# Performance work log

Measured on AMD Instinct MI355X. Metric: run time of the kernel, lower is better.

## Reference

```python
import jax, jax.numpy as jnp
import numpy as np


def median_pool8(x):
    # x: (N, 1, H0, W0); 8x8 non-overlapping blocks, lower median (torch.median semantics)
    N, C, H0, W0 = x.shape
    H, W = H0 // 8, W0 // 8
    blocks = x.reshape(N, C, H, 8, W, 8).transpose(0, 1, 2, 4, 3, 5).reshape(N, C, H, W, 64)
    return jnp.sort(blocks, axis=-1)[..., (64 - 1) // 2]


def prelu(x, a):
    return jnp.where(x >= 0, x, a * x)


def setup_inputs() -> dict:
    key = jax.random.key(0)
    ks = jax.random.split(key, 12)
    N, C, H, W = 8, 128, 45, 60
    s = 0.05
    return {
        "cnn_encoder_output": jax.random.normal(ks[0], (N, C, H, W), jnp.float32),
        "original_input": jax.random.uniform(ks[1], (N, 4, H * 8, W * 8), jnp.float32),
        "xy": jax.random.normal(ks[2], (N, 2, H * 8, W * 8), jnp.float32),
        # g MLP: two Linear(128,128) + PReLU (single alpha each)
        "g_w0": jax.random.normal(ks[3], (C, C), jnp.float32) * s,
        "g_b0": jnp.zeros((C,), jnp.float32),
        "g_a0": jnp.full((1,), 0.25, jnp.float32),
        "g_w1": jax.random.normal(ks[4], (C, C), jnp.float32) * s,
        "g_b1": jnp.zeros((C,), jnp.float32),
        "g_a1": jnp.full((1,), 0.25, jnp.float32),
        # q update: Linear(256,128) + PReLU
        "q_w": jax.random.normal(ks[5], (C, 2 * C), jnp.float32) * s,
        "q_b": jnp.zeros((C,), jnp.float32),
        "q_a": jnp.full((1,), 0.25, jnp.float32),
        # output conv: Conv2d(256, 128, 3, padding=1)
        "conv_w": jax.random.normal(ks[6], (C, 2 * C, 3, 3), jnp.float32) * s,
        "conv_b": jnp.zeros((C,), jnp.float32),
        "gnn_iterations": 2,
        "k": 16,
        "use_half_precision": 0,
    }


def reference(cnn_encoder_output, original_input, xy,
              g_w0, g_b0, g_a0, g_w1, g_b1, g_a1,
              q_w, q_b, q_a, conv_w, conv_b,
              gnn_iterations, k, use_half_precision):
    N, C, H, W = cnn_encoder_output.shape
    HW = H * W

    # 3D projection: median-pooled x, y, depth -> (N, HW, 3)
    depth = median_pool8(original_input[:, 3:4])
    xc = median_pool8(xy[:, 0:1])
    yc = median_pool8(xy[:, 1:2])
    proj = jnp.concatenate([xc, yc, depth], axis=1).reshape(N, 3, HW).transpose(0, 2, 1)

    # batched KNN: D_ij = sqrt(|pi|^2 + |pj|^2 - 2 pi.pj), k smallest per row
    sq = jnp.sum(proj * proj, axis=-1)                        # (N, HW)
    r = jnp.einsum('nic,njc->nij', proj, proj)                # (N, HW, HW)
    D = jnp.sqrt(jnp.maximum(sq[:, :, None] + sq[:, None, :] - 2.0 * r, 0.0))
    _, knn = jax.lax.top_k(-D, k)                             # (N, HW, K) indices

    h = cnn_encoder_output.transpose(0, 2, 3, 1).reshape(N, HW, C)
    g_params = [(g_w0, g_b0, g_a0), (g_w1, g_b1, g_a1)]

    for _ in range(gnn_iterations):
        # gather neighbor features: (N, HW, K, C)
        nf = jax.vmap(lambda hn, kn: hn[kn])(h, knn)
        for w, b, a in g_params:
            nf = prelu(nf @ w.T + b, a)
        m = jnp.mean(nf, axis=2)                              # (N, HW, C)
        h = prelu(jnp.concatenate([h, m], axis=-1) @ q_w.T + q_b, q_a)

    h_img = h.reshape(N, H, W, C).transpose(0, 3, 1, 2)
    inp = jnp.concatenate([cnn_encoder_output, h_img], axis=1)  # (N, 2C, H, W)
    out = jax.lax.conv_general_dilated(
        inp, conv_w, window_strides=(1, 1), padding=((1, 1), (1, 1)),
        dimension_numbers=('NCHW', 'OIHW', 'NCHW')) + conv_b[None, :, None, None]
    return out
```

## Files before the change

### kernel.cpp

```cpp
#include <hip/hip_runtime.h>
#include <cfloat>
#include <cmath>

#define NB 8
#define CC 128
#define HH 45
#define WW 60
#define HWP 2700
#define KNN 16
#define H0 360
#define W0 480
#define NT 43
#define MROWS 21600

typedef __bf16 bf16_8 __attribute__((ext_vector_type(8)));
typedef __bf16 bf16_4 __attribute__((ext_vector_type(4)));
typedef float  f32x4  __attribute__((ext_vector_type(4)));

__global__ void transpose_cl(const float* __restrict__ in, __bf16* __restrict__ cnn_b,
                             __bf16* __restrict__ pad_in) {
    __shared__ float tile[32][33];
    int n = blockIdx.z;
    int c0 = blockIdx.y * 32;
    int p0 = blockIdx.x * 32;
    int tx = threadIdx.x & 31, ty = threadIdx.x >> 5;
    #pragma unroll
    for (int r = 0; r < 32; r += 8) {
        int c = c0 + ty + r, p = p0 + tx;
        tile[ty + r][tx] = (p < HWP) ? in[((size_t)n * CC + c) * HWP + p] : 0.f;
    }
    __syncthreads();
    #pragma unroll
    for (int r = 0; r < 32; r += 8) {
        int p = p0 + ty + r, c = c0 + tx;
        if (p < HWP) {
            __bf16 bv = (__bf16)tile[tx][ty + r];
            cnn_b[((size_t)n * HWP + p) * 128 + c] = bv;
            int y = p / WW, x = p % WW;
            pad_in[(((size_t)n * 47 + y + 1) * 68 + (x + 1)) * 256 + c] = bv;
        }
    }
}

__global__ void median_pool(const float* __restrict__ xy, const float* __restrict__ orig,
                            float* __restrict__ proj) {
    int w = blockIdx.x * 4 + (threadIdx.x >> 6);
    int lane = threadIdx.x & 63;
    int n = w / (3 * HWP);
    int rem = w % (3 * HWP);
    int c = rem / HWP;
    int b = rem % HWP;
    const float* src = (c < 2) ? (xy + ((size_t)n * 2 + c) * H0 * W0)
                               : (orig + ((size_t)n * 4 + 3) * H0 * W0);
    int by = b / WW, bx = b % WW;
    int r = lane >> 3, col = lane & 7;
    float v = src[(by * 8 + r) * W0 + bx * 8 + col];
    #pragma unroll
    for (int k = 2; k <= 64; k <<= 1) {
        #pragma unroll
        for (int j2 = k >> 1; j2 >= 1; j2 >>= 1) {
            float p = __shfl_xor(v, j2, 64);
            bool dir = (lane & k) == 0;
            bool low = (lane & j2) == 0;
            v = (dir == low) ? fminf(v, p) : fmaxf(v, p);
        }
    }
    if (lane == 31) proj[(size_t)c * (NB * HWP) + (size_t)n * HWP + b] = v;
}

__global__ void __launch_bounds__(512, 6) knn_kernel(const float* __restrict__ proj,
                                                     int* __restrict__ knn) {
#pragma clang fp contract(off)
    __shared__ float4 pts[HWP];
    __shared__ int sbufj[8][64];
    __shared__ int scnt[8];
    int n = blockIdx.y;
    const float* px = proj + (size_t)n * HWP;
    const float* py = proj + (size_t)NB * HWP + (size_t)n * HWP;
    const float* pz = proj + (size_t)2 * NB * HWP + (size_t)n * HWP;
    for (int t = threadIdx.x; t < HWP; t += 512) {
        float x = px[t], y = py[t], z = pz[t];
        float4 p;
        p.x = x; p.y = y; p.z = z;
        p.w = (x * x + y * y) + z * z;
        pts[t] = p;
    }
    __syncthreads();

    int wave = threadIdx.x >> 6;
    int lane = threadIdx.x & 63;
    int i = blockIdx.x * 8 + wave;
    if (i >= HWP) return;
    float4 pi = pts[i];
    float xi = pi.x, yi = pi.y, zi = pi.z, sqi = pi.w;

    unsigned int sdp[22];
    float mn = FLT_MAX;
    #pragma unroll
    for (int t = 0; t < NT; ++t) {
        int j = lane + t * 64;
        unsigned int u = 0xFFFFu;
        if (j < HWP) {
            float4 pj = pts[j];
            float r = fmaf(zi, pj.z, fmaf(yi, pj.y, xi * pj.x));
            float s = (sqi + pj.w) - 2.0f * r;
            mn = fminf(mn, s);
            float sc = fmaxf(s, 0.f);
            u = (__float_as_uint(sc) + 0xFFFFu) >> 16;
        }
        if (t & 1) sdp[t >> 1] |= (u << 16);
        else       sdp[t >> 1] = u;
    }

    float v = mn;
    #pragma unroll
    for (int k = 2; k <= 64; k <<= 1) {
        #pragma unroll
        for (int j2 = k >> 1; j2 >= 1; j2 >>= 1) {
            float p = __shfl_xor(v, j2, 64);
            bool dir = (lane & k) == 0;
            bool low = (lane & j2) == 0;
            v = (dir == low) ? fminf(v, p) : fmaxf(v, p);
        }
    }
    float M_s = __shfl(v, 15, 64);
    float M_test = (M_s > 0.f) ? (M_s * 1.0000005f + 1e-37f) : 0.0f;
    float M_t2 = M_test * 1.009f;
    unsigned int M_bits = __float_as_uint(M_t2);

    if (lane == 0) scnt[wave] = 0;
    #pragma unroll
    for (int t = 0; t < NT; ++t) {
        unsigned int u = (t & 1) ? (sdp[t >> 1] >> 16) : (sdp[t >> 1] & 0xFFFFu);
        bool pred = (u << 16) <= M_bits;
        if (pred) {
            int slot = atomicAdd(&scnt[wave], 1);
            if (slot < 64) sbufj[wave][slot] = lane + t * 64;
        }
    }
    int cnt = scnt[wave];

    int myj = 0;
    if (cnt >= KNN && cnt <= 64) {
        unsigned long long key = ~0ull;
        if (lane < cnt) {
            int j = sbufj[wave][lane];
            float4 pj = pts[j];
            float r = fmaf(zi, pj.z, fmaf(yi, pj.y, xi * pj.x));
            float s = (sqi + pj.w) - 2.0f * r;
            float d = sqrtf(fmaxf(s, 0.f));
            key = ((unsigned long long)__float_as_uint(d) << 32) | (unsigned int)j;
        }
        #pragma unroll
        for (int k = 2; k <= 64; k <<= 1) {
            #pragma unroll
            for (int j2 = k >> 1; j2 >= 1; j2 >>= 1) {
                unsigned long long p = __shfl_xor(key, j2, 64);
                bool dir = (lane & k) == 0;
                bool low = (lane & j2) == 0;
                bool keepmin = (dir == low);
                bool pless = p < key;
                key = (pless == keepmin) ? p : key;
            }
        }
        myj = (int)(unsigned int)(key & 0xffffffffull);
    } else {
        float lastd = -FLT_MAX; int lastj = -1;
        #pragma unroll 1
        for (int r = 0; r < KNN; ++r) {
            float bd = FLT_MAX; int bj = 0x7fffffff;
            #pragma unroll 1
            for (int t = 0; t < NT; ++t) {
                int j = lane + t * 64;
                if (j < HWP) {
                    float4 pj = pts[j];
                    float rr = fmaf(zi, pj.z, fmaf(yi, pj.y, xi * pj.x));
                    float s = (sqi + pj.w) - 2.0f * rr;
                    float d = sqrtf(fmaxf(s, 0.f));
                    bool gt = (d > lastd) || (d == lastd && j > lastj);
                    bool lt = (d < bd) || (d == bd && j < bj);
                    if (gt && lt) { bd = d; bj = j; }
                }
            }
            float md = bd; int mj = bj;
            #pragma unroll
            for (int off = 32; off >= 1; off >>= 1) {
                float od = __shfl_xor(md, off, 64);
                int oj = __shfl_xor(mj, off, 64);
                if (od < md || (od == md && oj < mj)) { md = od; mj = oj; }
            }
            if (lane == r) myj = mj;
            lastd = md; lastj = mj;
        }
    }
    if (lane < KNN)
        knn[((size_t)n * HWP + i) * KNN + lane] = myj;
}

template <int K>
__device__ __forceinline__ void wfrag_body(const float* __restrict__ Wt,
                                           __bf16* __restrict__ wf, int bx, int tid) {
    int t = bx * 256 + tid;
    int j = t & 7;
    int lane = (t >> 3) & 63;
    int nt = (t >> 9) & 7;
    int kc = t >> 12;
    int oc = nt * 16 + (lane & 15);
    int k = kc * 32 + (lane >> 4) * 8 + j;
    wf[t] = (__bf16)Wt[(size_t)oc * K + k];
}

__global__ void prep_all(const float* __restrict__ g_w0, const float* __restrict__ g_w1,
                         const float* __restrict__ q_w, const float* __restrict__ conv_w,
                         __bf16* __restrict__ g0f, __bf16* __restrict__ g1f,
                         __bf16* __restrict__ qf, __bf16* __restrict__ w_frag) {
    int bx = blockIdx.x, tid = threadIdx.x;
    if (bx < 64)        wfrag_body<128>(g_w0, g0f, bx, tid);
    else if (bx < 128)  wfrag_body<128>(g_w1, g1f, bx - 64, tid);
    else if (bx < 256)  wfrag_body<256>(q_w, qf, bx - 128, tid);
    else {
        int t = (bx - 256) * 256 + tid;
        int j = t & 7;
        int lane = (t >> 3) & 63;
        int ntile = (t >> 9) & 7;
        int icc = (t >> 12) & 7;
        int tap = t >> 15;
        int oc = ntile * 16 + (lane & 15);
        int ic = icc * 32 + (lane >> 4) * 8 + j;
        w_frag[t] = (__bf16)conv_w[((size_t)oc * 256 + ic) * 9 + tap];
    }
}

__device__ __forceinline__ void layer_b(
    const __bf16* __restrict__ src,
    const __bf16* __restrict__ wf,
    int wave, int lane, int kc_base, f32x4 acc[2][2]) {
    int quad = lane >> 4, lm = lane & 15;
    const bf16_8* wf8 = (const bf16_8*)wf;
    #pragma unroll
    for (int kc = 0; kc < 4; ++kc) {
        bf16_8 b[2], a[2];
        #pragma unroll
        for (int nt = 0; nt < 2; ++nt)
            b[nt] = *(const bf16_8*)&src[(nt * 16 + lm) * 136 + kc * 32 + quad * 8];
        #pragma unroll
        for (int mt = 0; mt < 2; ++mt)
            a[mt] = wf8[((size_t)(kc_base + kc) * 8 + (wave * 2 + mt)) * 64 + lane];
        #pragma unroll
        for (int mt = 0; mt < 2; ++mt)
            #pragma unroll
            for (int nt = 0; nt < 2; ++nt)
                acc[mt][nt] = __builtin_amdgcn_mfma_f32_16x16x32_bf16(
                    a[mt], b[nt], acc[mt][nt], 0, 0, 0);
    }
}

__global__ void __launch_bounds__(256) fused_g(
    const __bf16* __restrict__ Ain,
    const __bf16* __restrict__ w0f, const float* __restrict__ b0, const float* __restrict__ a0p,
    const __bf16* __restrict__ w1f, const float* __restrict__ b1, const float* __restrict__ a1p,
    __bf16* __restrict__ tgb) {
    __shared__ __bf16 albuf[32 * 136];
    __shared__ __bf16 inter[32 * 136];
    int r0 = blockIdx.x * 32;
    int tid = threadIdx.x;
    int wave = tid >> 6, lane = tid & 63;
    int quad = lane >> 4, lm = lane & 15;
    #pragma unroll
    for (int t = tid; t < 512; t += 256) {
        int row = t >> 4, c8 = (t & 15) * 8;
        *(bf16_8*)&albuf[row * 136 + c8] =
            *(const bf16_8*)&Ain[(size_t)(r0 + row) * 128 + c8];
    }
    __syncthreads();
    {
        f32x4 acc[2][2] = {};
        layer_b(albuf, w0f, wave, lane, 0, acc);
        float alpha = a0p[0];
        #pragma unroll
        for (int mt = 0; mt < 2; ++mt) {
            int oc0 = wave * 32 + mt * 16 + quad * 4;
            float4 bb = *(const float4*)&b0[oc0];
            float bv[4] = {bb.x, bb.y, bb.z, bb.w};
            #pragma unroll
            for (int nt = 0; nt < 2; ++nt) {
                bf16_4 o;
                #pragma unroll
                for (int reg = 0; reg < 4; ++reg) {
                    float vv = acc[mt][nt][reg] + bv[reg];
                    vv = (vv >= 0.f) ? vv : alpha * vv;
                    o[reg] = (__bf16)vv;
                }
                *(bf16_4*)&inter[(nt * 16 + lm) * 136 + oc0] = o;
            }
        }
    }
    __syncthreads();
    {
        f32x4 acc[2][2] = {};
        layer_b(inter, w1f, wave, lane, 0, acc);
        float alpha = a1p[0];
        #pragma unroll
        for (int mt = 0; mt < 2; ++mt) {
            int oc0 = wave * 32 + mt * 16 + quad * 4;
            float4 bb = *(const float4*)&b1[oc0];
            float bv[4] = {bb.x, bb.y, bb.z, bb.w};
            #pragma unroll
            for (int nt = 0; nt < 2; ++nt) {
                bf16_4 o;
                #pragma unroll
                for (int reg = 0; reg < 4; ++reg) {
                    float vv = acc[mt][nt][reg] + bv[reg];
                    vv = (vv >= 0.f) ? vv : alpha * vv;
                    o[reg] = (__bf16)vv;
                }
                *(bf16_4*)&tgb[(size_t)(r0 + nt * 16 + lm) * 128 + oc0] = o;
            }
        }
    }
}

__global__ void __launch_bounds__(256) fused_q(
    const __bf16* __restrict__ Ain, const __bf16* __restrict__ tgb,
    const int* __restrict__ knn_idx,
    const __bf16* __restrict__ qf, const float* __restrict__ qb,
    const float* __restrict__ qap,
    __bf16* __restrict__ out_lin, __bf16* __restrict__ pad_out, int mode) {
    __shared__ __bf16 hlds[32 * 136];
    __shared__ __bf16 mlds[32 * 136];
    int r0 = blockIdx.x * 32;
    int tid = threadIdx.x;
    int wave = tid >> 6, lane = tid & 63;
    int quad = lane >> 4, lm = lane & 15;
    #pragma unroll
    for (int t = tid; t < 512; t += 256) {
        int row = t >> 4, c8 = (t & 15) * 8;
        *(bf16_8*)&hlds[row * 136 + c8] =
            *(const bf16_8*)&Ain[(size_t)(r0 + row) * 128 + c8];
    }
    {
        int pix = tid >> 3;
        int oct0 = (tid & 7) * 2;
        int grow = r0 + pix;
        int nimg = grow / HWP;
        const int* kn = knn_idx + (size_t)grow * KNN;
        const __bf16* tbase = tgb + ((size_t)nimg * HWP) * 128;
        float a0[8] = {}, a1[8] = {};
        #pragma unroll
        for (int k = 0; k < KNN; ++k) {
            int j = kn[k];
            const __bf16* srcp = tbase + (size_t)j * 128 + oct0 * 8;
            bf16_8 v0 = *(const bf16_8*)srcp;
            bf16_8 v1 = *(const bf16_8*)(srcp + 8);
            #pragma unroll
            for (int e = 0; e < 8; ++e) { a0[e] += (float)v0[e]; a1[e] += (float)v1[e]; }
        }
        const float s = 1.f / 16.f;
        bf16_8 o0, o1;
        #pragma unroll
        for (int e = 0; e < 8; ++e) { o0[e] = (__bf16)(a0[e] * s); o1[e] = (__bf16)(a1[e] * s); }
        *(bf16_8*)&mlds[pix * 136 + oct0 * 8] = o0;
        *(bf16_8*)&mlds[pix * 136 + oct0 * 8 + 8] = o1;
    }
    __syncthreads();
    f32x4 acc[2][2] = {};
    layer_b(hlds, qf, wave, lane, 0, acc);
    layer_b(mlds, qf, wave, lane, 4, acc);
    float alpha = qap[0];
    #pragma unroll
    for (int mt = 0; mt < 2; ++mt) {
        int oc0 = wave * 32 + mt * 16 + quad * 4;
        float4 bb = *(const float4*)&qb[oc0];
        float bv[4] = {bb.x, bb.y, bb.z, bb.w};
        #pragma unroll
        for (int nt = 0; nt < 2; ++nt) {
            bf16_4 o;
            #pragma unroll
            for (int reg = 0; reg < 4; ++reg) {
                float vv = acc[mt][nt][reg] + bv[reg];
                vv = (vv >= 0.f) ? vv : alpha * vv;
                o[reg] = (__bf16)vv;
            }
            int grow = r0 + nt * 16 + lm;
            if (mode == 0) {
                *(bf16_4*)&out_lin[(size_t)grow * 128 + oc0] = o;
            } else {
                int n = grow / HWP, p = grow % HWP;
                int y = p / WW, x = p % WW;
                *(bf16_4*)&pad_out[(((size_t)n * 47 + y + 1) * 68 + (x + 1)) * 256 + 128 + oc0] = o;
            }
        }
    }
}

__global__ void zero_border(__bf16* __restrict__ pad_in) {
    int t = blockIdx.x * 256 + threadIdx.x;
    int cg = t & 31;
    int s = t >> 5;
    int cell = s % 496;
    int n = s / 496;
    int y, x;
    if (cell < 136) { y = (cell < 68) ? 0 : 46; x = cell % 68; }
    else {
        int rem = cell - 136;
        y = 1 + rem / 8;
        int k = rem % 8;
        x = (k == 0) ? 0 : (60 + k);
    }
    bf16_8 z = {};
    *(bf16_8*)&pad_in[(((size_t)n * 47 + y) * 68 + x) * 256 + cg * 8] = z;
}

__global__ void __launch_bounds__(256) conv_mfma(
    const __bf16* __restrict__ pad_in,
    const __bf16* __restrict__ w_frag,
    const float* __restrict__ bias,
    float* __restrict__ out) {
    __shared__ __bf16 alds[3 * 66 * 32];
    int y = blockIdx.x;
    int oh = blockIdx.y;
    int n = blockIdx.z;
    int tid = threadIdx.x;
    int wave = tid >> 6, lane = tid & 63;
    int wm = wave & 1, wq = wave >> 1;
    int quad = lane >> 4, lm = lane & 15;

    f32x4 acc[2][2] = {};
    const bf16_8* wf = (const bf16_8*)w_frag;

    for (int icc = 0; icc < 8; ++icc) {
        __syncthreads();
        for (int t = tid; t < 792; t += 256) {
            int cq = t & 3;
            int xp = (t >> 2) % 66;
            int dy = (t >> 2) / 66;
            size_t src = (((size_t)n * 47 + (y + dy)) * 68 + xp) * 256 + icc * 32 + cq * 8;
            *(bf16_8*)&alds[(dy * 66 + xp) * 32 + cq * 8] = *(const bf16_8*)&pad_in[src];
        }
        __syncthreads();
        #pragma unroll
        for (int tap = 0; tap < 9; ++tap) {
            int ky = tap / 3, kx = tap % 3;
            bf16_8 b[2], a[2];
            #pragma unroll
            for (int nt = 0; nt < 2; ++nt)
                b[nt] = wf[(((tap * 8 + icc) * 8) + (oh * 4 + wq * 2 + nt)) * 64 + lane];
            #pragma unroll
            for (int mt = 0; mt < 2; ++mt)
                a[mt] = *(const bf16_8*)&alds[(ky * 66 + (wm * 32 + mt * 16 + lm + kx)) * 32 + quad * 8];
            #pragma unroll
            for (int mt = 0; mt < 2; ++mt)
                #pragma unroll
                for (int nt = 0; nt < 2; ++nt)
                    acc[mt][nt] = __builtin_amdgcn_mfma_f32_16x16x32_bf16(
                        a[mt], b[nt], acc[mt][nt], 0, 0, 0);
        }
    }
    #pragma unroll
    for (int mt = 0; mt < 2; ++mt) {
        int x0 = wm * 32 + mt * 16 + quad * 4;
        if (x0 >= WW) continue;
        #pragma unroll
        for (int nt = 0; nt < 2; ++nt) {
            int oc = (oh * 4 + wq * 2 + nt) * 16 + lm;
            float bb = bias[oc];
            f32x4 v = acc[mt][nt];
            v[0] += bb; v[1] += bb; v[2] += bb; v[3] += bb;
            *(f32x4*)&out[(((size_t)n * 128 + oc) * HH + y) * WW + x0] = v;
        }
    }
}

extern "C" void kernel_launch(void* const* d_in, const int* in_sizes, int n_in,
                              void* d_out, int out_size, void* d_ws, size_t ws_size,
                              hipStream_t stream) {
    const float* cnn    = (const float*)d_in[0];
    const float* orig   = (const float*)d_in[1];
    const float* xy     = (const float*)d_in[2];
    const float* g_w0   = (const float*)d_in[3];
    const float* g_b0   = (const float*)d_in[4];
    const float* g_a0   = (const float*)d_in[5];
    const float* g_w1   = (const float*)d_in[6];
    const float* g_b1   = (const float*)d_in[7];
    const float* g_a1   = (const float*)d_in[8];
    const float* q_w    = (const float*)d_in[9];
    const float* q_b    = (const float*)d_in[10];
    const float* q_a    = (const float*)d_in[11];
    const float* conv_w = (const float*)d_in[12];
    const float* conv_b = (const float*)d_in[13];
    float* out = (float*)d_out;

    float* ws = (float*)d_ws;
    const size_t SB = (size_t)MROWS * 128;
    __bf16* cnn_b  = (__bf16*)ws;
    __bf16* h_b    = cnn_b + SB;
    __bf16* tgb    = h_b + SB;
    float*  proj   = (float*)(tgb + SB);
    int*    knn_i  = (int*)(proj + 64800);
    __bf16* g0f    = (__bf16*)(knn_i + (size_t)MROWS * KNN);
    __bf16* g1f    = g0f + 16384;
    __bf16* qf     = g1f + 16384;
    __bf16* w_frag = qf + 32768;
    __bf16* pad_in = w_frag + 294912;

    transpose_cl<<<dim3(85, 4, NB), 256, 0, stream>>>(cnn, cnn_b, pad_in);
    median_pool<<<16200, 256, 0, stream>>>(xy, orig, proj);
    knn_kernel<<<dim3(338, NB), 512, 0, stream>>>(proj, knn_i);
    prep_all<<<1408, 256, 0, stream>>>(g_w0, g_w1, q_w, conv_w, g0f, g1f, qf, w_frag);
    zero_border<<<496, 256, 0, stream>>>(pad_in);

    fused_g<<<675, 256, 0, stream>>>(cnn_b, g0f, g_b0, g_a0, g1f, g_b1, g_a1, tgb);
    fused_q<<<675, 256, 0, stream>>>(cnn_b, tgb, knn_i, qf, q_b, q_a, h_b, pad_in, 0);

    fused_g<<<675, 256, 0, stream>>>(h_b, g0f, g_b0, g_a0, g1f, g_b1, g_a1, tgb);
    fused_q<<<675, 256, 0, stream>>>(h_b, tgb, knn_i, qf, q_b, q_a, h_b, pad_in, 1);

    conv_mfma<<<dim3(HH, 2, NB), 256, 0, stream>>>(pad_in, w_frag, conv_b, out);
}
```

Before: 254.0 us.

## Merge setup kernels into one launch and widen conv channel staging

Folds the transpose, median pool, weight-fragment prep and border-zero kernels into one launch, with block-index ranges selecting the job. This removes three kernel launches and their gaps. The conv kernel now stages 64 channels per pass into a padded shared-memory row of 72, which halves the number of sync/load rounds but uses more LDS. The KNN candidate test now compares 16-bit keys directly instead of shifting them back up.

Measured after the change: 244.1 us. -3.9%, faster.

```diff
diff --git a/kernel.cpp b/kernel.cpp
--- a/kernel.cpp
+++ b/kernel.cpp
@@ -17,55 +17,109 @@
 typedef __bf16 bf16_4 __attribute__((ext_vector_type(4)));
 typedef float  f32x4  __attribute__((ext_vector_type(4)));
 
-__global__ void transpose_cl(const float* __restrict__ in, __bf16* __restrict__ cnn_b,
-                             __bf16* __restrict__ pad_in) {
-    __shared__ float tile[32][33];
-    int n = blockIdx.z;
-    int c0 = blockIdx.y * 32;
-    int p0 = blockIdx.x * 32;
-    int tx = threadIdx.x & 31, ty = threadIdx.x >> 5;
-    #pragma unroll
-    for (int r = 0; r < 32; r += 8) {
-        int c = c0 + ty + r, p = p0 + tx;
-        tile[ty + r][tx] = (p < HWP) ? in[((size_t)n * CC + c) * HWP + p] : 0.f;
-    }
-    __syncthreads();
-    #pragma unroll
-    for (int r = 0; r < 32; r += 8) {
-        int p = p0 + ty + r, c = c0 + tx;
-        if (p < HWP) {
-            __bf16 bv = (__bf16)tile[tx][ty + r];
-            cnn_b[((size_t)n * HWP + p) * 128 + c] = bv;
-            int y = p / WW, x = p % WW;
-            pad_in[(((size_t)n * 47 + y + 1) * 68 + (x + 1)) * 256 + c] = bv;
-        }
-    }
-}
-
-__global__ void median_pool(const float* __restrict__ xy, const float* __restrict__ orig,
-                            float* __restrict__ proj) {
-    int w = blockIdx.x * 4 + (threadIdx.x >> 6);
-    int lane = threadIdx.x & 63;
-    int n = w / (3 * HWP);
-    int rem = w % (3 * HWP);
-    int c = rem / HWP;
-    int b = rem % HWP;
-    const float* src = (c < 2) ? (xy + ((size_t)n * 2 + c) * H0 * W0)
-                               : (orig + ((size_t)n * 4 + 3) * H0 * W0);
-    int by = b / WW, bx = b % WW;
-    int r = lane >> 3, col = lane & 7;
-    float v = src[(by * 8 + r) * W0 + bx * 8 + col];
-    #pragma unroll
-    for (int k = 2; k <= 64; k <<= 1) {
-        #pragma unroll
-        for (int j2 = k >> 1; j2 >= 1; j2 >>= 1) {
-            float p = __shfl_xor(v, j2, 64);
-            bool dir = (lane & k) == 0;
-            bool low = (lane & j2) == 0;
-            v = (dir == low) ? fminf(v, p) : fmaxf(v, p);
-        }
-    }
-    if (lane == 31) proj[(size_t)c * (NB * HWP) + (size_t)n * HWP + b] = v;
+template <int K>
+__device__ __forceinline__ void wfrag_body(const float* __restrict__ Wt,
+                                           __bf16* __restrict__ wf, int bx, int tid) {
+    int t = bx * 256 + tid;
+    int j = t & 7;
+    int lane = (t >> 3) & 63;
+    int nt = (t >> 9) & 7;
+    int kc = t >> 12;
+    int oc = nt * 16 + (lane & 15);
+    int k = kc * 32 + (lane >> 4) * 8 + j;
+    wf[t] = (__bf16)Wt[(size_t)oc * K + k];
+}
+
+__global__ void __launch_bounds__(256) setup_all(
+    const float* __restrict__ cnn, const float* __restrict__ xy,
+    const float* __restrict__ orig,
+    const float* __restrict__ g_w0, const float* __restrict__ g_w1,
+    const float* __restrict__ q_w, const float* __restrict__ conv_w,
+    __bf16* __restrict__ cnn_b, __bf16* __restrict__ pad_in,
+    float* __restrict__ proj,
+    __bf16* __restrict__ g0f, __bf16* __restrict__ g1f,
+    __bf16* __restrict__ qf, __bf16* __restrict__ w_frag) {
+    int bx = blockIdx.x;
+    int tid = threadIdx.x;
+    if (bx < 2720) {
+        __shared__ float tile[32][33];
+        int n = bx / 340;
+        int r2 = bx % 340;
+        int c0 = (r2 / 85) * 32;
+        int p0 = (r2 % 85) * 32;
+        int tx = tid & 31, ty = tid >> 5;
+        #pragma unroll
+        for (int r = 0; r < 32; r += 8) {
+            int c = c0 + ty + r, p = p0 + tx;
+            tile[ty + r][tx] = (p < HWP) ? cnn[((size_t)n * CC + c) * HWP + p] : 0.f;
+        }
+        __syncthreads();
+        #pragma unroll
+        for (int r = 0; r < 32; r += 8) {
+            int p = p0 + ty + r, c = c0 + tx;
+            if (p < HWP) {
+                __bf16 bv = (__bf16)tile[tx][ty + r];
+                cnn_b[((size_t)n * HWP + p) * 128 + c] = bv;
+                int y = p / WW, x = p % WW;
+                pad_in[(((size_t)n * 47 + y + 1) * 68 + (x + 1)) * 256 + c] = bv;
+            }
+        }
+    } else if (bx < 2720 + 16200) {
+        int w = (bx - 2720) * 4 + (tid >> 6);
+        int lane = tid & 63;
+        int n = w / (3 * HWP);
+        int rem = w % (3 * HWP);
+        int c = rem / HWP;
+        int b = rem % HWP;
+        const float* src = (c < 2) ? (xy + ((size_t)n * 2 + c) * H0 * W0)
+                                   : (orig + ((size_t)n * 4 + 3) * H0 * W0);
+        int by = b / WW, bxp = b % WW;
+        int r = lane >> 3, col = lane & 7;
+        float v = src[(by * 8 + r) * W0 + bxp * 8 + col];
+        #pragma unroll
+        for (int k = 2; k <= 64; k <<= 1) {
+            #pragma unroll
+            for (int j2 = k >> 1; j2 >= 1; j2 >>= 1) {
+                float p = __shfl_xor(v, j2, 64);
+                bool dir = (lane & k) == 0;
+                bool low = (lane & j2) == 0;
+                v = (dir == low) ? fminf(v, p) : fmaxf(v, p);
+            }
+        }
+        if (lane == 31) proj[(size_t)c * (NB * HWP) + (size_t)n * HWP + b] = v;
+    } else if (bx < 2720 + 16200 + 1408) {
+        int pb = bx - (2720 + 16200);
+        if (pb < 64)        wfrag_body<128>(g_w0, g0f, pb, tid);
+        else if (pb < 128)  wfrag_body<128>(g_w1, g1f, pb - 64, tid);
+        else if (pb < 256)  wfrag_body<256>(q_w, qf, pb - 128, tid);
+        else {
+            int t = (pb - 256) * 256 + tid;
+            int j = t & 7;
+            int lane = (t >> 3) & 63;
+            int ntile = (t >> 9) & 7;
+            int icc = (t >> 12) & 7;
+            int tap = t >> 15;
+            int oc = ntile * 16 + (lane & 15);
+            int ic = icc * 32 + (lane >> 4) * 8 + j;
+            w_frag[t] = (__bf16)conv_w[((size_t)oc * 256 + ic) * 9 + tap];
+        }
+    } else {
+        int t = (bx - (2720 + 16200 + 1408)) * 256 + tid;
+        int cg = t & 31;
+        int s = t >> 5;
+        int cell = s % 496;
+        int n = s / 496;
+        int y, x;
+        if (cell < 136) { y = (cell < 68) ? 0 : 46; x = cell % 68; }
+        else {
+            int rem = cell - 136;
+            y = 1 + rem / 8;
+            int k = rem % 8;
+            x = (k == 0) ? 0 : (60 + k);
+        }
+        bf16_8 z = {};
+        *(bf16_8*)&pad_in[(((size_t)n * 47 + y) * 68 + x) * 256 + cg * 8] = z;
+    }
 }
 
 __global__ void __launch_bounds__(512, 6) knn_kernel(const float* __restrict__ proj,
@@ -126,14 +180,13 @@
     float M_s = __shfl(v, 15, 64);
     float M_test = (M_s > 0.f) ? (M_s * 1.0000005f + 1e-37f) : 0.0f;
     float M_t2 = M_test * 1.009f;
-    unsigned int M_bits = __float_as_uint(M_t2);
+    unsigned int M16 = __float_as_uint(M_t2) >> 16;
 
     if (lane == 0) scnt[wave] = 0;
     #pragma unroll
     for (int t = 0; t < NT; ++t) {
         unsigned int u = (t & 1) ? (sdp[t >> 1] >> 16) : (sdp[t >> 1] & 0xFFFFu);
-        bool pred = (u << 16) <= M_bits;
-        if (pred) {
+        if (u <= M16) {
             int slot = atomicAdd(&scnt[wave], 1);
             if (slot < 64) sbufj[wave][slot] = lane + t * 64;
         }
@@ -197,40 +250,6 @@
         knn[((size_t)n * HWP + i) * KNN + lane] = myj;
 }
 
-template <int K>
-__device__ __forceinline__ void wfrag_body(const float* __restrict__ Wt,
-                                           __bf16* __restrict__ wf, int bx, int tid) {
-    int t = bx * 256 + tid;
-    int j = t & 7;
-    int lane = (t >> 3) & 63;
-    int nt = (t >> 9) & 7;
-    int kc = t >> 12;
-    int oc = nt * 16 + (lane & 15);
-    int k = kc * 32 + (lane >> 4) * 8 + j;
-    wf[t] = (__bf16)Wt[(size_t)oc * K + k];
-}
-
-__global__ void prep_all(const float* __restrict__ g_w0, const float* __restrict__ g_w1,
-                         const float* __restrict__ q_w, const float* __restrict__ conv_w,
-                         __bf16* __restrict__ g0f, __bf16* __restrict__ g1f,
-                         __bf16* __restrict__ qf, __bf16* __restrict__ w_frag) {
-    int bx = blockIdx.x, tid = threadIdx.x;
-    if (bx < 64)        wfrag_body<128>(g_w0, g0f, bx, tid);
-    else if (bx < 128)  wfrag_body<128>(g_w1, g1f, bx - 64, tid);
-    else if (bx < 256)  wfrag_body<256>(q_w, qf, bx - 128, tid);
-    else {
-        int t = (bx - 256) * 256 + tid;
-        int j = t & 7;
-        int lane = (t >> 3) & 63;
-        int ntile = (t >> 9) & 7;
-        int icc = (t >> 12) & 7;
-        int tap = t >> 15;
-        int oc = ntile * 16 + (lane & 15);
-        int ic = icc * 32 + (lane >> 4) * 8 + j;
-        w_frag[t] = (__bf16)conv_w[((size_t)oc * 256 + ic) * 9 + tap];
-    }
-}
-
 __device__ __forceinline__ void layer_b(
     const __bf16* __restrict__ src,
     const __bf16* __restrict__ wf,
@@ -393,30 +412,12 @@
     }
 }
 
-__global__ void zero_border(__bf16* __restrict__ pad_in) {
-    int t = blockIdx.x * 256 + threadIdx.x;
-    int cg = t & 31;
-    int s = t >> 5;
-    int cell = s % 496;
-    int n = s / 496;
-    int y, x;
-    if (cell < 136) { y = (cell < 68) ? 0 : 46; x = cell % 68; }
-    else {
-        int rem = cell - 136;
-        y = 1 + rem / 8;
-        int k = rem % 8;
-        x = (k == 0) ? 0 : (60 + k);
-    }
-    bf16_8 z = {};
-    *(bf16_8*)&pad_in[(((size_t)n * 47 + y) * 68 + x) * 256 + cg * 8] = z;
-}
-
 __global__ void __launch_bounds__(256) conv_mfma(
     const __bf16* __restrict__ pad_in,
     const __bf16* __restrict__ w_frag,
     const float* __restrict__ bias,
     float* __restrict__ out) {
-    __shared__ __bf16 alds[3 * 66 * 32];
+    __shared__ __bf16 alds[3 * 66 * 72];
     int y = blockIdx.x;
     int oh = blockIdx.y;
     int n = blockIdx.z;
@@ -428,32 +429,37 @@
     f32x4 acc[2][2] = {};
     const bf16_8* wf = (const bf16_8*)w_frag;
 
-    for (int icc = 0; icc < 8; ++icc) {
+    for (int c64 = 0; c64 < 4; ++c64) {
         __syncthreads();
-        for (int t = tid; t < 792; t += 256) {
-            int cq = t & 3;
-            int xp = (t >> 2) % 66;
-            int dy = (t >> 2) / 66;
-            size_t src = (((size_t)n * 47 + (y + dy)) * 68 + xp) * 256 + icc * 32 + cq * 8;
-            *(bf16_8*)&alds[(dy * 66 + xp) * 32 + cq * 8] = *(const bf16_8*)&pad_in[src];
+        for (int t = tid; t < 1584; t += 256) {
+            int cq = t & 7;
+            int xp = (t >> 3) % 66;
+            int dy = (t >> 3) / 66;
+            size_t src = (((size_t)n * 47 + (y + dy)) * 68 + xp) * 256 + c64 * 64 + cq * 8;
+            *(bf16_8*)&alds[(dy * 66 + xp) * 72 + cq * 8] = *(const bf16_8*)&pad_in[src];
         }
         __syncthreads();
         #pragma unroll
         for (int tap = 0; tap < 9; ++tap) {
             int ky = tap / 3, kx = tap % 3;
-            bf16_8 b[2], a[2];
-            #pragma unroll
-            for (int nt = 0; nt < 2; ++nt)
-                b[nt] = wf[(((tap * 8 + icc) * 8) + (oh * 4 + wq * 2 + nt)) * 64 + lane];
-            #pragma unroll
-            for (int mt = 0; mt < 2; ++mt)
-                a[mt] = *(const bf16_8*)&alds[(ky * 66 + (wm * 32 + mt * 16 + lm + kx)) * 32 + quad * 8];
-            #pragma unroll
-            for (int mt = 0; mt < 2; ++mt)
+            #pragma unroll
+            for (int h = 0; h < 2; ++h) {
+                int icc = c64 * 2 + h;
+                bf16_8 b[2], a[2];
                 #pragma unroll
                 for (int nt = 0; nt < 2; ++nt)
-                    acc[mt][nt] = __builtin_amdgcn_mfma_f32_16x16x32_bf16(
-                        a[mt], b[nt], acc[mt][nt], 0, 0, 0);
+                    b[nt] = wf[(((tap * 8 + icc) * 8) + (oh * 4 + wq * 2 + nt)) * 64 + lane];
+                #pragma unroll
+                for (int mt = 0; mt < 2; ++mt)
+                    a[mt] = *(const bf16_8*)&alds[(ky * 66 + (wm * 32 + mt * 16 + lm + kx)) * 72
+                                                  + h * 32 + quad * 8];
+                #pragma unroll
+                for (int mt = 0; mt < 2; ++mt)
+                    #pragma unroll
+                    for (int nt = 0; nt < 2; ++nt)
+                        acc[mt][nt] = __builtin_amdgcn_mfma_f32_16x16x32_bf16(
+                            a[mt], b[nt], acc[mt][nt], 0, 0, 0);
+            }
         }
     }
     #pragma unroll
@@ -503,11 +509,10 @@
     __bf16* w_frag = qf + 32768;
     __bf16* pad_in = w_frag + 294912;
 
-    transpose_cl<<<dim3(85, 4, NB), 256, 0, stream>>>(cnn, cnn_b, pad_in);
-    median_pool<<<16200, 256, 0, stream>>>(xy, orig, proj);
+    setup_all<<<2720 + 16200 + 1408 + 496, 256, 0, stream>>>(
+        cnn, xy, orig, g_w0, g_w1, q_w, conv_w,
+        cnn_b, pad_in, proj, g0f, g1f, qf, w_frag);
     knn_kernel<<<dim3(338, NB), 512, 0, stream>>>(proj, knn_i);
-    prep_all<<<1408, 256, 0, stream>>>(g_w0, g_w1, q_w, conv_w, g0f, g1f, qf, w_frag);
-    zero_border<<<496, 256, 0, stream>>>(pad_in);
 
     fused_g<<<675, 256, 0, stream>>>(cnn_b, g0f, g_b0, g_a0, g1f, g_b1, g_a1, tgb);
     fused_q<<<675, 256, 0, stream>>>(cnn_b, tgb, knn_i, qf, q_b, q_a, h_b, pad_in, 0);
```
